# Optimization experiments

Hardware: AMD Instinct MI355X
Metric: run time of the kernel (lower is better)

The kernel has to match this reference:

```python
import jax, jax.numpy as jnp
import numpy as np
from jax import lax

B, L, D = 2, 1024, 1024
INTER = 2816  # _find_multiple(round(4.0*1024*2/3), 256)
K, PAD = 3, 1
S = 32  # sqrt(L)
K2 = K * K


def setup_inputs() -> dict:
    key = jax.random.key(0)
    ks = jax.random.split(key, 7)
    x = jax.random.normal(ks[0], (B, L, D), dtype=jnp.float32)
    w_gate_up = jax.random.normal(ks[1], (2 * INTER, D), dtype=jnp.float32) / np.sqrt(D)
    w_metric = jax.random.normal(ks[2], (7, INTER, 3, 3), dtype=jnp.float32) / np.sqrt(INTER * 9)
    b_metric = jax.random.normal(ks[3], (7,), dtype=jnp.float32) * 0.01
    conv_w = jax.random.normal(ks[4], (INTER, 1, K, K), dtype=jnp.float32) / K
    conv_b = jnp.zeros((INTER,), dtype=jnp.float32)
    w_down = jax.random.normal(ks[5], (D, INTER), dtype=jnp.float32) / np.sqrt(INTER)
    return {"x": x, "w_gate_up": w_gate_up, "w_metric": w_metric,
            "b_metric": b_metric, "conv_w": conv_w, "conv_b": conv_b,
            "w_down": w_down}


def _metric_offsets(x2d, w_metric, b_metric):
    # Finsler-Randers style metric: 2x2 linear map M, drift vector, tanh scale.
    p = lax.conv_general_dilated(x2d, w_metric, (1, 1), 'SAME',
                                 dimension_numbers=('NCHW', 'OIHW', 'NCHW'))
    p = p + b_metric[None, :, None, None]  # [B,7,S,S]
    m00, m01, m10, m11 = p[:, 0], p[:, 1], p[:, 2], p[:, 3]
    dr_y, dr_x = p[:, 4], p[:, 5]
    scale = jnp.tanh(p[:, 6])
    ky = (jnp.arange(K) - PAD).astype(x2d.dtype)
    py = jnp.repeat(ky, K)   # (K2,) kernel-tap dy
    px = jnp.tile(ky, K)     # (K2,) kernel-tap dx
    pyb = py[None, :, None, None]
    pxb = px[None, :, None, None]
    off_y = scale[:, None] * (m00[:, None] * pyb + m01[:, None] * pxb) + dr_y[:, None]
    off_x = scale[:, None] * (m10[:, None] * pyb + m11[:, None] * pxb) + dr_x[:, None]
    return off_y, off_x, py, px  # offsets: [B,K2,S,S]


def _deform_depthwise(x2d, off_y, off_x, py, px, conv_w, conv_b):
    # Sampling positions per output pixel & kernel tap: [B,K2,S,S]
    iy = jnp.arange(S, dtype=x2d.dtype)
    pos_y = iy[None, None, :, None] + py[None, :, None, None] + off_y
    pos_x = iy[None, None, None, :] + px[None, :, None, None] + off_x
    y0 = jnp.floor(pos_y)
    x0 = jnp.floor(pos_x)
    ty = pos_y - y0
    tx = pos_x - x0
    y0i = y0.astype(jnp.int32)
    x0i = x0.astype(jnp.int32)
    flat = x2d.reshape(B, INTER, S * S)

    def corner(yy, xx):
        valid = ((yy >= 0) & (yy < S) & (xx >= 0) & (xx < S)).astype(x2d.dtype)
        idx = (jnp.clip(yy, 0, S - 1) * S + jnp.clip(xx, 0, S - 1)).reshape(B, 1, -1)
        v = jnp.take_along_axis(flat, idx, axis=2).reshape(B, INTER, K2, S, S)
        return v * valid[:, None]

    w00 = ((1 - ty) * (1 - tx))[:, None]
    w01 = ((1 - ty) * tx)[:, None]
    w10 = (ty * (1 - tx))[:, None]
    w11 = (ty * tx)[:, None]
    acc = w00 * corner(y0i, x0i)
    acc = acc + w01 * corner(y0i, x0i + 1)
    acc = acc + w10 * corner(y0i + 1, x0i)
    acc = acc + w11 * corner(y0i + 1, x0i + 1)
    out = jnp.einsum('bckij,ck->bcij', acc, conv_w.reshape(INTER, K2))
    return out + conv_b[None, :, None, None]


def reference(x, w_gate_up, w_metric, b_metric, conv_w, conv_b, w_down):
    gu = jnp.einsum('bld,fd->blf', x, w_gate_up)          # [B,L,2*inter]
    gate, up = jnp.split(gu, 2, axis=-1)
    x_ffn = jax.nn.silu(gate) * up                         # [B,L,inter]
    x2d = x_ffn.transpose(0, 2, 1).reshape(B, INTER, S, S)
    off_y, off_x, py, px = _metric_offsets(x2d, w_metric, b_metric)
    out2d = _deform_depthwise(x2d, off_y, off_x, py, px, conv_w, conv_b)
    grid_out = out2d.reshape(B, INTER, L).transpose(0, 2, 1)
    return jnp.einsum('blf,df->bld', grid_out, w_down)
```

## Files before the change

### kernel.cpp

```cpp
#include <hip/hip_runtime.h>
#include <hip/hip_bf16.h>
#include <hip/hip_fp16.h>
#include <cstdint>
#include <cstddef>
#include <type_traits>

#define INTER 2816

typedef __bf16 bf16x8 __attribute__((ext_vector_type(8)));
typedef _Float16 f16x8 __attribute__((ext_vector_type(8)));
typedef float f32x4 __attribute__((ext_vector_type(4)));
typedef unsigned short u16x8 __attribute__((ext_vector_type(8)));
using bf16 = __hip_bfloat16;
using u16 = unsigned short;

__device__ __forceinline__ u16 f2bu(float f) {
  bf16 h = __float2bfloat16(f);
  return *reinterpret_cast<u16*>(&h);
}
__device__ __forceinline__ u16 f2hu(float f) {
  __half h = __float2half(f);
  return *reinterpret_cast<u16*>(&h);
}

__device__ __forceinline__ void async16(const u16* g, u16* l) {
  __builtin_amdgcn_global_load_lds(
      (const __attribute__((address_space(1))) unsigned int*)g,
      (__attribute__((address_space(3))) unsigned int*)l, 16, 0, 0);
}

template <bool H>
__device__ __forceinline__ void stage8(u16* dst, const float* src) {
  const float4 a = *(const float4*)(src);
  const float4 b = *(const float4*)(src + 4);
  u16 tmp[8];
  if constexpr (H) {
    tmp[0] = f2hu(a.x); tmp[1] = f2hu(a.y); tmp[2] = f2hu(a.z); tmp[3] = f2hu(a.w);
    tmp[4] = f2hu(b.x); tmp[5] = f2hu(b.y); tmp[6] = f2hu(b.z); tmp[7] = f2hu(b.w);
  } else {
    tmp[0] = f2bu(a.x); tmp[1] = f2bu(a.y); tmp[2] = f2bu(a.z); tmp[3] = f2bu(a.w);
    tmp[4] = f2bu(b.x); tmp[5] = f2bu(b.y); tmp[6] = f2bu(b.z); tmp[7] = f2bu(b.w);
  }
  *(uint4*)dst = *(uint4*)tmp;
}

__global__ __launch_bounds__(256)
void prep_all(const float* __restrict__ x, const float* __restrict__ wgu,
              const float* __restrict__ wd, const float* __restrict__ w_metric,
              const float* __restrict__ conv_w, u16* __restrict__ xbf,
              u16* __restrict__ wgubf, u16* __restrict__ wdbf,
              u16* __restrict__ wm2, u16* __restrict__ cwb) {
  constexpr size_t S0 = (size_t)2048 * 1024;
  constexpr size_t S1 = (size_t)5632 * 1024;
  constexpr size_t S2 = (size_t)1024 * 2816;
  constexpr size_t NCONV_THREADS = (S0 + S1 + S2) / 8;
  const size_t t = (size_t)blockIdx.x * 256 + threadIdx.x;
  if (t < NCONV_THREADS) {
    const size_t e0 = t * 8;
    if (e0 < S0) {
      stage8<false>(xbf + e0, x + e0);
    } else if (e0 < S0 + S1) {
      stage8<false>(wgubf + (e0 - S0), wgu + (e0 - S0));
    } else {
      stage8<true>(wdbf + (e0 - S0 - S1), wd + (e0 - S0 - S1));
    }
  } else {
    const unsigned p = (unsigned)(t - NCONV_THREADS);
    const unsigned y = p / 2816u;
    const unsigned c = p - y * 2816u;
    if (y < 64) {
      float v = 0.f;
      if (y < 63) {
        const unsigned o = y / 9, tap = y - o * 9;
        v = w_metric[((size_t)o * INTER + c) * 9 + tap];
      }
      wm2[(size_t)y * INTER + c] = f2hu(v);
    } else {
      const unsigned k = y - 64;
      cwb[(size_t)k * INTER + c] = f2hu(conv_w[(size_t)c * 9 + k]);
    }
  }
}

template <int BN, bool NSWAP, typename OT>
__global__ __launch_bounds__(256, 3)
void gemm_nt(const u16* __restrict__ A, int lda, const u16* __restrict__ Bt,
             int ldb, OT* __restrict__ C, int M, int ldc, int K) {
  constexpr int NJ = BN / 32;
  constexpr int BHALF = BN * 32;
  __shared__ u16 As[2 * 128 * 32];
  __shared__ u16 Bs[2 * BHALF];
  const size_t koff = (size_t)blockIdx.z * K;
  A += koff;
  Bt += koff;
  C += (size_t)blockIdx.z * M * ldc;
  const int m0 = (NSWAP ? blockIdx.y : blockIdx.x) * 128;
  const int n0 = (NSWAP ? blockIdx.x : blockIdx.y) * BN;
  const int tid = threadIdx.x;
  const int lane = tid & 63;
  const int wv = tid >> 6;
  const int wm = wv & 1, wn = wv >> 1;
  const int lr = lane & 15;
  const int lq = lane >> 4;

  f32x4 acc[4][NJ];
#pragma unroll
  for (int i = 0; i < 4; ++i)
#pragma unroll
    for (int j = 0; j < NJ; ++j) acc[i][j] = (f32x4){0.f, 0.f, 0.f, 0.f};

  const int srow = tid >> 2;
  const int scol = (tid & 3) * 8;
  const u16* gA0 = A + (size_t)(m0 + srow) * lda + scol;
  const u16* gA1 = A + (size_t)(m0 + 64 + srow) * lda + scol;
  const u16* gB0 = Bt + (size_t)(n0 + srow) * ldb + scol;
  const u16* gB1 = Bt + (size_t)(n0 + 64 + srow) * ldb + scol;

  for (int kb = 0; kb < K; kb += 64) {
#pragma unroll
    for (int h = 0; h < 2; ++h) {
      const int kh = kb + h * 32;
      async16(gA0 + kh, As + h * 4096 + tid * 8);
      async16(gA1 + kh, As + h * 4096 + 2048 + tid * 8);
      async16(gB0 + kh, Bs + h * BHALF + tid * 8);
      if constexpr (BN == 128) async16(gB1 + kh, Bs + h * BHALF + 2048 + tid * 8);
    }
    __syncthreads();
#pragma unroll
    for (int h = 0; h < 2; ++h) {
      f16x8 af[4], bfr[NJ];
#pragma unroll
      for (int i = 0; i < 4; ++i)
        af[i] = *(const f16x8*)(&As[h * 4096 + (wm * 64 + i * 16 + lr) * 32 + lq * 8]);
#pragma unroll
      for (int j = 0; j < NJ; ++j)
        bfr[j] = *(const f16x8*)(&Bs[h * BHALF + (wn * (BN / 2) + j * 16 + lr) * 32 + lq * 8]);
#pragma unroll
      for (int i = 0; i < 4; ++i)
#pragma unroll
        for (int j = 0; j < NJ; ++j)
          acc[i][j] = __builtin_amdgcn_mfma_f32_16x16x32_f16(af[i], bfr[j],
                                                             acc[i][j], 0, 0, 0);
    }
    __syncthreads();
  }

#pragma unroll
  for (int i = 0; i < 4; ++i)
#pragma unroll
    for (int j = 0; j < NJ; ++j) {
      const int col = n0 + wn * (BN / 2) + j * 16 + lr;
#pragma unroll
      for (int r = 0; r < 4; ++r) {
        const int row = m0 + wm * 64 + i * 16 + lq * 4 + r;
        const float v = acc[i][j][r];
        if constexpr (std::is_same_v<OT, float>) {
          C[(size_t)row * ldc + col] = v;
        } else {
          C[(size_t)row * ldc + col] = f2hu(v);
        }
      }
    }
}

__global__ void reduce4(const float* __restrict__ q2, float* __restrict__ out) {
  const size_t i = ((size_t)blockIdx.x * 256 + threadIdx.x) * 4;
  const size_t S = (size_t)2048 * 1024;
  float4 a = *(const float4*)(q2 + i);
  const float4 b = *(const float4*)(q2 + S + i);
  const float4 c = *(const float4*)(q2 + 2 * S + i);
  const float4 d = *(const float4*)(q2 + 3 * S + i);
  a.x += b.x + c.x + d.x;
  a.y += b.y + c.y + d.y;
  a.z += b.z + c.z + d.z;
  a.w += b.w + c.w + d.w;
  *(float4*)(out + i) = a;
}

__global__ __launch_bounds__(256)
void presum11(const float* __restrict__ q, float* __restrict__ qsum) {
  const size_t i = ((size_t)blockIdx.x * 256 + threadIdx.x) * 4;
  float4 s = *(const float4*)(q + i);
#pragma unroll
  for (int ks = 1; ks < 11; ++ks) {
    const float4 v = *(const float4*)(q + (size_t)ks * 131072 + i);
    s.x += v.x; s.y += v.y; s.z += v.z; s.w += v.w;
  }
  *(float4*)(qsum + i) = s;
}

__global__ __launch_bounds__(256, 3)
void gateup_gemm(const u16* __restrict__ x, const u16* __restrict__ wgu,
                 u16* __restrict__ xffn) {
  constexpr int K = 1024;
  __shared__ u16 As[2 * 128 * 32];
  __shared__ u16 Bgs[2 * 64 * 32];
  __shared__ u16 Bus[2 * 64 * 32];
  const int n0 = blockIdx.x * 64;
  const int m0 = blockIdx.y * 128;
  const int tid = threadIdx.x;
  const int lane = tid & 63;
  const int wv = tid >> 6;
  const int wm = wv & 1, wn = wv >> 1;
  const int lr = lane & 15;
  const int lq = lane >> 4;

  f32x4 accg[4][2], accu[4][2];
#pragma unroll
  for (int i = 0; i < 4; ++i)
#pragma unroll
    for (int j = 0; j < 2; ++j) {
      accg[i][j] = (f32x4){0.f, 0.f, 0.f, 0.f};
      accu[i][j] = (f32x4){0.f, 0.f, 0.f, 0.f};
    }

  const int srow = tid >> 2;
  const int scol = (tid & 3) * 8;
  const u16* gA0 = x + (size_t)(m0 + srow) * K + scol;
  const u16* gA1 = x + (size_t)(m0 + 64 + srow) * K + scol;
  const u16* gBg = wgu + (size_t)(n0 + srow) * K + scol;
  const u16* gBu = wgu + (size_t)(INTER + n0 + srow) * K + scol;

  for (int kb = 0; kb < K; kb += 64) {
#pragma unroll
    for (int h = 0; h < 2; ++h) {
      const int kh = kb + h * 32;
      async16(gA0 + kh, As + h * 4096 + tid * 8);
      async16(gA1 + kh, As + h * 4096 + 2048 + tid * 8);
      async16(gBg + kh, Bgs + h * 2048 + tid * 8);
      async16(gBu + kh, Bus + h * 2048 + tid * 8);
    }
    __syncthreads();
#pragma unroll
    for (int h = 0; h < 2; ++h) {
      bf16x8 af[4], bg[2], bu[2];
#pragma unroll
      for (int i = 0; i < 4; ++i)
        af[i] = *(const bf16x8*)(&As[h * 4096 + (wm * 64 + i * 16 + lr) * 32 + lq * 8]);
#pragma unroll
      for (int j = 0; j < 2; ++j) {
        bg[j] = *(const bf16x8*)(&Bgs[h * 2048 + (wn * 32 + j * 16 + lr) * 32 + lq * 8]);
        bu[j] = *(const bf16x8*)(&Bus[h * 2048 + (wn * 32 + j * 16 + lr) * 32 + lq * 8]);
      }
#pragma unroll
      for (int i = 0; i < 4; ++i)
#pragma unroll
        for (int j = 0; j < 2; ++j) {
          accg[i][j] = __builtin_amdgcn_mfma_f32_16x16x32_bf16(af[i], bg[j],
                                                               accg[i][j], 0, 0, 0);
          accu[i][j] = __builtin_amdgcn_mfma_f32_16x16x32_bf16(af[i], bu[j],
                                                               accu[i][j], 0, 0, 0);
        }
    }
    __syncthreads();
  }

#pragma unroll
  for (int i = 0; i < 4; ++i)
#pragma unroll
    for (int j = 0; j < 2; ++j) {
      const int col = n0 + wn * 32 + j * 16 + lr;
#pragma unroll
      for (int r = 0; r < 4; ++r) {
        const int row = m0 + wm * 64 + i * 16 + lq * 4 + r;
        const float g = accg[i][j][r];
        const float u = accu[i][j][r];
        const float s = g / (1.f + __expf(-g));
        xffn[(size_t)row * INTER + col] = f2hu(s * u);
      }
    }
}

__global__ __launch_bounds__(256)
void offsets_fused(const float* __restrict__ qsum,
                   const float* __restrict__ b_metric,
                   float4* __restrict__ wrec, int4* __restrict__ orec) {
  __shared__ float lds[130 * 65];
  const int chunk = blockIdx.x;
  const int b = chunk >> 4;
  const int c0 = (chunk & 15) * 64;
  const int t = threadIdx.x;

  for (int v = t; v < 130 * 16; v += 256) {
    const int row = v >> 4;
    const int c4 = (v & 15) * 4;
    int pg = c0 - 33 + row;
    pg = min(max(pg, 0), 1023);
    const float4 s = *(const float4*)(qsum + ((size_t)b * 1024 + pg) * 64 + c4);
    float* d = &lds[row * 65 + c4];
    d[0] = s.x; d[1] = s.y; d[2] = s.z; d[3] = s.w;
  }
  __syncthreads();
  if (t >= 64) return;

  const int pix = c0 + t;
  const int i = pix >> 5, j = pix & 31;
  float p[7];
#pragma unroll
  for (int o = 0; o < 7; ++o) p[o] = b_metric[o];
#pragma unroll
  for (int tap = 0; tap < 9; ++tap) {
    const int dy = tap / 3 - 1, dx = tap % 3 - 1;
    const int ii = i + dy, jj = j + dx;
    if ((unsigned)ii < 32u && (unsigned)jj < 32u) {
      const float* r = &lds[(t + 33 + dy * 32 + dx) * 65 + tap];
#pragma unroll
      for (int o = 0; o < 7; ++o) p[o] += r[o * 9];
    }
  }
  const float m00 = p[0], m01 = p[1], m10 = p[2], m11 = p[3];
  const float dry = p[4], drx = p[5];
  const float sc = tanhf(p[6]);
#pragma unroll
  for (int k = 0; k < 9; ++k) {
    const float pyk = (float)(k / 3 - 1), pxk = (float)(k % 3 - 1);
    const float offy = sc * (m00 * pyk + m01 * pxk) + dry;
    const float offx = sc * (m10 * pyk + m11 * pxk) + drx;
    const float posy = (float)i + pyk + offy;
    const float posx = (float)j + pxk + offx;
    const float y0f = floorf(posy), x0f = floorf(posx);
    const int y0 = (int)y0f, x0 = (int)x0f;
    const float ty = posy - y0f, tx = posx - x0f;
    const int y1 = y0 + 1, x1 = x0 + 1;
    const float vy0 = ((unsigned)y0 < 32u) ? 1.f : 0.f;
    const float vy1 = ((unsigned)y1 < 32u) ? 1.f : 0.f;
    const float vx0 = ((unsigned)x0 < 32u) ? 1.f : 0.f;
    const float vx1 = ((unsigned)x1 < 32u) ? 1.f : 0.f;
    float4 w;
    w.x = (1.f - ty) * (1.f - tx) * vy0 * vx0;
    w.y = (1.f - ty) * tx * vy0 * vx1;
    w.z = ty * (1.f - tx) * vy1 * vx0;
    w.w = ty * tx * vy1 * vx1;
    const int cy0 = min(max(y0, 0), 31), cy1 = min(max(y1, 0), 31);
    const int cx0 = min(max(x0, 0), 31), cx1 = min(max(x1, 0), 31);
    int4 o;
    o.x = (cy0 * 32 + cx0) * (INTER * 2);
    o.y = (cy0 * 32 + cx1) * (INTER * 2);
    o.z = (cy1 * 32 + cx0) * (INTER * 2);
    o.w = (cy1 * 32 + cx1) * (INTER * 2);
    const size_t r = (((size_t)b * 9 + k) << 10) + pix;
    wrec[r] = w;
    orec[r] = o;
  }
}

__global__ __launch_bounds__(256)
void deform_kernel(const u16* __restrict__ xffn,
                   const float4* __restrict__ wrec,
                   const int4* __restrict__ orec,
                   const u16* __restrict__ cwb,
                   const float* __restrict__ conv_b,
                   u16* __restrict__ gridout) {
  __shared__ float4 sw[2][9];
  __shared__ int4 so[2][9];
  const unsigned bid = (blockIdx.x & 7u) * 352u + (blockIdx.x >> 3);
  const unsigned t0 = bid * 256;
  const unsigned p0 = t0 / 352u;
  const unsigned t = t0 + threadIdx.x;
  const unsigned pix = t / 352u;
  const unsigned cv = t - pix * 352u;
  const int c0 = cv * 8;
  const int b = pix >> 10, l = pix & 1023;

  if (threadIdx.x < 36) {
    const int pp = threadIdx.x / 18;
    const int rr = threadIdx.x - pp * 18;
    const int k = (rr < 9) ? rr : rr - 9;
    const unsigned pixel = p0 + pp;
    if (pixel < 2048) {
      const int bb = pixel >> 10, ll = pixel & 1023;
      const size_t r = (((size_t)bb * 9 + k) << 10) + ll;
      if (rr < 9) sw[pp][k] = wrec[r];
      else        so[pp][k] = orec[r];
    }
  }
  __syncthreads();

  const int pp = (int)(pix - p0);

  union U8 { u16x8 u; __half2 h[4]; uint4 q; };

  __half2 acc2[4];
  {
    const float4 b0 = *(const float4*)(&conv_b[c0]);
    const float4 b1 = *(const float4*)(&conv_b[c0 + 4]);
    acc2[0] = __floats2half2_rn(b0.x, b0.y);
    acc2[1] = __floats2half2_rn(b0.z, b0.w);
    acc2[2] = __floats2half2_rn(b1.x, b1.y);
    acc2[3] = __floats2half2_rn(b1.z, b1.w);
  }
  const char* xb = (const char*)xffn +
                   ((size_t)b * 1024 * INTER + c0) * sizeof(u16);
#pragma unroll
  for (int k = 0; k < 9; ++k) {
    const float4 w = sw[pp][k];
    const int4 o = so[pp][k];
    const __half2 wx = __float2half2_rn(w.x);
    const __half2 wy = __float2half2_rn(w.y);
    const __half2 wz = __float2half2_rn(w.z);
    const __half2 ww = __float2half2_rn(w.w);
    U8 v00, v01, v10, v11, cw;
    v00.u = *(const u16x8*)(xb + o.x);
    v01.u = *(const u16x8*)(xb + o.y);
    v10.u = *(const u16x8*)(xb + o.z);
    v11.u = *(const u16x8*)(xb + o.w);
    cw.u = *(const u16x8*)(&cwb[(size_t)k * INTER + c0]);
#pragma unroll
    for (int p = 0; p < 4; ++p) {
      __half2 bl = __hmul2(wx, v00.h[p]);
      bl = __hfma2(wy, v01.h[p], bl);
      bl = __hfma2(wz, v10.h[p], bl);
      bl = __hfma2(ww, v11.h[p], bl);
      acc2[p] = __hfma2(bl, cw.h[p], acc2[p]);
    }
  }
  U8 outv;
#pragma unroll
  for (int p = 0; p < 4; ++p) outv.h[p] = acc2[p];
  *(uint4*)(gridout + ((size_t)b * 1024 + l) * INTER + c0) = outv.q;
}

extern "C" void kernel_launch(void* const* d_in, const int* in_sizes, int n_in,
                              void* d_out, int out_size, void* d_ws,
                              size_t ws_size, hipStream_t stream) {
  const float* x         = (const float*)d_in[0];
  const float* w_gate_up = (const float*)d_in[1];
  const float* w_metric  = (const float*)d_in[2];
  const float* b_metric  = (const float*)d_in[3];
  const float* conv_w    = (const float*)d_in[4];
  const float* conv_b    = (const float*)d_in[5];
  const float* w_down    = (const float*)d_in[6];
  float* out = (float*)d_out;

  char* w = (char*)d_ws;
  u16* gridout  = (u16*)(w);
  float* q2     = (float*)(w + (12u << 20));
  u16* xffn     = (u16*)(w + (12u << 20));
  u16* xbf      = (u16*)(w + (24u << 20));
  u16* wgubf    = (u16*)(w + (28u << 20) + (256u << 10));
  float* q_conv = (float*)(w + (28u << 20) + (256u << 10));
  float* qsum   = (float*)(w + (36u << 20));
  u16* wm2      = (u16*)(w + (40u << 20));
  u16* cwb      = (u16*)(w + (41u << 20));
  float4* wrec  = (float4*)(w + (42u << 20));
  int4* orec    = (int4*)(w + (43u << 20));
  u16* wdbf     = (u16*)(w + (44u << 20));

  prep_all<<<6051, 256, 0, stream>>>(x, w_gate_up, w_down, w_metric, conv_w,
                                     xbf, wgubf, wdbf, wm2, cwb);
  gateup_gemm<<<dim3(44, 16), 256, 0, stream>>>(xbf, wgubf, xffn);
  gemm_nt<64, false, float><<<dim3(16, 1, 11), 256, 0, stream>>>(
      xffn, INTER, wm2, INTER, q_conv, 2048, 64, 256);
  presum11<<<128, 256, 0, stream>>>(q_conv, qsum);
  offsets_fused<<<32, 256, 0, stream>>>(qsum, b_metric, wrec, orec);
  deform_kernel<<<2816, 256, 0, stream>>>(xffn, wrec, orec, cwb, conv_b,
                                          gridout);
  gemm_nt<128, true, float><<<dim3(8, 16, 4), 256, 0, stream>>>(
      gridout, INTER, wdbf, INTER, q2, 2048, 1024, 704);
  reduce4<<<2048, 256, 0, stream>>>(q2, out);
}
```

Baseline: 190.5 us.

## Double-buffer async LDS loads in both GEMM kernels to overlap copy with MFMA

```diff
diff --git a/kernel.cpp b/kernel.cpp
--- a/kernel.cpp
+++ b/kernel.cpp
@@ -116,33 +116,45 @@
   const u16* gB0 = Bt + (size_t)(n0 + srow) * ldb + scol;
   const u16* gB1 = Bt + (size_t)(n0 + 64 + srow) * ldb + scol;
 
-  for (int kb = 0; kb < K; kb += 64) {
-#pragma unroll
-    for (int h = 0; h < 2; ++h) {
-      const int kh = kb + h * 32;
-      async16(gA0 + kh, As + h * 4096 + tid * 8);
-      async16(gA1 + kh, As + h * 4096 + 2048 + tid * 8);
-      async16(gB0 + kh, Bs + h * BHALF + tid * 8);
-      if constexpr (BN == 128) async16(gB1 + kh, Bs + h * BHALF + 2048 + tid * 8);
-    }
-    __syncthreads();
-#pragma unroll
-    for (int h = 0; h < 2; ++h) {
-      f16x8 af[4], bfr[NJ];
-#pragma unroll
-      for (int i = 0; i < 4; ++i)
-        af[i] = *(const f16x8*)(&As[h * 4096 + (wm * 64 + i * 16 + lr) * 32 + lq * 8]);
+  auto stage = [&](int kh, int bi) {
+    async16(gA0 + kh, As + bi * 4096 + tid * 8);
+    async16(gA1 + kh, As + bi * 4096 + 2048 + tid * 8);
+    async16(gB0 + kh, Bs + bi * BHALF + tid * 8);
+    if constexpr (BN == 128) async16(gB1 + kh, Bs + bi * BHALF + 2048 + tid * 8);
+  };
+
+  const int nh = K >> 5;
+  stage(0, 0);
+
+  for (int hh = 0; hh < nh; ++hh) {
+    const int p = hh & 1;
+    if (hh + 1 < nh) {
+      stage((hh + 1) * 32, p ^ 1);
+      if constexpr (BN == 128)
+        asm volatile("s_waitcnt vmcnt(4)" ::: "memory");
+      else
+        asm volatile("s_waitcnt vmcnt(3)" ::: "memory");
+    } else {
+      asm volatile("s_waitcnt vmcnt(0)" ::: "memory");
+    }
+    __builtin_amdgcn_s_barrier();
+    __builtin_amdgcn_sched_barrier(0);
+
+    f16x8 af[4], bfr[NJ];
+#pragma unroll
+    for (int i = 0; i < 4; ++i)
+      af[i] = *(const f16x8*)(&As[p * 4096 + (wm * 64 + i * 16 + lr) * 32 + lq * 8]);
+#pragma unroll
+    for (int j = 0; j < NJ; ++j)
+      bfr[j] = *(const f16x8*)(&Bs[p * BHALF + (wn * (BN / 2) + j * 16 + lr) * 32 + lq * 8]);
+#pragma unroll
+    for (int i = 0; i < 4; ++i)
 #pragma unroll
       for (int j = 0; j < NJ; ++j)
-        bfr[j] = *(const f16x8*)(&Bs[h * BHALF + (wn * (BN / 2) + j * 16 + lr) * 32 + lq * 8]);
-#pragma unroll
-      for (int i = 0; i < 4; ++i)
-#pragma unroll
-        for (int j = 0; j < NJ; ++j)
-          acc[i][j] = __builtin_amdgcn_mfma_f32_16x16x32_f16(af[i], bfr[j],
-                                                             acc[i][j], 0, 0, 0);
-    }
-    __syncthreads();
+        acc[i][j] = __builtin_amdgcn_mfma_f32_16x16x32_f16(af[i], bfr[j],
+                                                           acc[i][j], 0, 0, 0);
+    __builtin_amdgcn_sched_barrier(0);
+    __builtin_amdgcn_s_barrier();
   }
 
 #pragma unroll
@@ -221,38 +233,47 @@
   const u16* gBg = wgu + (size_t)(n0 + srow) * K + scol;
   const u16* gBu = wgu + (size_t)(INTER + n0 + srow) * K + scol;
 
-  for (int kb = 0; kb < K; kb += 64) {
-#pragma unroll
-    for (int h = 0; h < 2; ++h) {
-      const int kh = kb + h * 32;
-      async16(gA0 + kh, As + h * 4096 + tid * 8);
-      async16(gA1 + kh, As + h * 4096 + 2048 + tid * 8);
-      async16(gBg + kh, Bgs + h * 2048 + tid * 8);
-      async16(gBu + kh, Bus + h * 2048 + tid * 8);
-    }
-    __syncthreads();
-#pragma unroll
-    for (int h = 0; h < 2; ++h) {
-      bf16x8 af[4], bg[2], bu[2];
-#pragma unroll
-      for (int i = 0; i < 4; ++i)
-        af[i] = *(const bf16x8*)(&As[h * 4096 + (wm * 64 + i * 16 + lr) * 32 + lq * 8]);
+  auto stage = [&](int kh, int bi) {
+    async16(gA0 + kh, As + bi * 4096 + tid * 8);
+    async16(gA1 + kh, As + bi * 4096 + 2048 + tid * 8);
+    async16(gBg + kh, Bgs + bi * 2048 + tid * 8);
+    async16(gBu + kh, Bus + bi * 2048 + tid * 8);
+  };
+
+  constexpr int NH = K >> 5;
+  stage(0, 0);
+
+  for (int hh = 0; hh < NH; ++hh) {
+    const int p = hh & 1;
+    if (hh + 1 < NH) {
+      stage((hh + 1) * 32, p ^ 1);
+      asm volatile("s_waitcnt vmcnt(4)" ::: "memory");
+    } else {
+      asm volatile("s_waitcnt vmcnt(0)" ::: "memory");
+    }
+    __builtin_amdgcn_s_barrier();
+    __builtin_amdgcn_sched_barrier(0);
+
+    bf16x8 af[4], bg[2], bu[2];
+#pragma unroll
+    for (int i = 0; i < 4; ++i)
+      af[i] = *(const bf16x8*)(&As[p * 4096 + (wm * 64 + i * 16 + lr) * 32 + lq * 8]);
+#pragma unroll
+    for (int j = 0; j < 2; ++j) {
+      bg[j] = *(const bf16x8*)(&Bgs[p * 2048 + (wn * 32 + j * 16 + lr) * 32 + lq * 8]);
+      bu[j] = *(const bf16x8*)(&Bus[p * 2048 + (wn * 32 + j * 16 + lr) * 32 + lq * 8]);
+    }
+#pragma unroll
+    for (int i = 0; i < 4; ++i)
 #pragma unroll
       for (int j = 0; j < 2; ++j) {
-        bg[j] = *(const bf16x8*)(&Bgs[h * 2048 + (wn * 32 + j * 16 + lr) * 32 + lq * 8]);
-        bu[j] = *(const bf16x8*)(&Bus[h * 2048 + (wn * 32 + j * 16 + lr) * 32 + lq * 8]);
+        accg[i][j] = __builtin_amdgcn_mfma_f32_16x16x32_bf16(af[i], bg[j],
+                                                             accg[i][j], 0, 0, 0);
+        accu[i][j] = __builtin_amdgcn_mfma_f32_16x16x32_bf16(af[i], bu[j],
+                                                             accu[i][j], 0, 0, 0);
       }
-#pragma unroll
-      for (int i = 0; i < 4; ++i)
-#pragma unroll
-        for (int j = 0; j < 2; ++j) {
-          accg[i][j] = __builtin_amdgcn_mfma_f32_16x16x32_bf16(af[i], bg[j],
-                                                               accg[i][j], 0, 0, 0);
-          accu[i][j] = __builtin_amdgcn_mfma_f32_16x16x32_bf16(af[i], bu[j],
-                                                               accu[i][j], 0, 0, 0);
-        }
-    }
-    __syncthreads();
+    __builtin_amdgcn_sched_barrier(0);
+    __builtin_amdgcn_s_barrier();
   }
 
 #pragma unroll
```

New measurement: 191.8 us. About the same (+0.7%).
